# Kernel tuning notes

Measured on AMD Instinct MI355X. Metric: run time of the kernel, lower is better.

The kernel has to match this reference:

```python
import jax, jax.numpy as jnp
import numpy as np

EMBED_DIM = 256
NUM_HEADS = 4
HEAD_DIM = EMBED_DIM // NUM_HEADS
B, H, W = 2, 64, 64


def _conv1x1(x, w, b):
    # x: [B,C,H,W], w: [O,C], b: [O] -> [B,O,H,W]
    return jnp.einsum('oc,bchw->bohw', w, x) + b[None, :, None, None]


def setup_inputs() -> dict:
    key = jax.random.key(0)
    ks = jax.random.split(key, 10)
    s = 1.0 / np.sqrt(EMBED_DIM)
    d = dict(
        x_q=jax.random.normal(ks[0], (B, EMBED_DIM, H, W), jnp.float32),
        x_kv=jax.random.normal(ks[1], (B, EMBED_DIM, H, W), jnp.float32),
        wq=jax.random.normal(ks[2], (EMBED_DIM, EMBED_DIM), jnp.float32) * s,
        bq=jax.random.normal(ks[3], (EMBED_DIM,), jnp.float32) * s,
        wk=jax.random.normal(ks[4], (EMBED_DIM, EMBED_DIM), jnp.float32) * s,
        bk=jax.random.normal(ks[5], (EMBED_DIM,), jnp.float32) * s,
        wv=jax.random.normal(ks[6], (EMBED_DIM, EMBED_DIM), jnp.float32) * s,
        bv=jax.random.normal(ks[7], (EMBED_DIM,), jnp.float32) * s,
        wo=jax.random.normal(ks[8], (EMBED_DIM, EMBED_DIM), jnp.float32) * s,
        bo=jax.random.normal(ks[9], (EMBED_DIM,), jnp.float32) * s,
    )
    return d


def reference(x_q, x_kv, wq, bq, wk, bk, wv, bv, wo, bo):
    b, c, h, w = x_q.shape
    scale = HEAD_DIM ** (-0.5)
    q = _conv1x1(x_q, wq, bq)
    k = _conv1x1(x_kv, wk, bk)
    v = _conv1x1(x_kv, wv, bv)
    s = h * w
    # [B, heads, head_dim, S]
    q = q.reshape(b, NUM_HEADS, HEAD_DIM, s)
    k = k.reshape(b, NUM_HEADS, HEAD_DIM, s)
    v = v.reshape(b, NUM_HEADS, HEAD_DIM, s)
    # attn[b,h,i,j] = sum_d q[b,h,d,i] * k[b,h,d,j]
    attn = jnp.einsum('bndi,bndj->bnij', q, k) * scale
    attn = jax.nn.softmax(attn, axis=-1)
    # out[b,h,i,d] = sum_j attn[b,h,i,j] * v[b,h,d,j]
    out = jnp.einsum('bnij,bndj->bnid', attn, v)
    out = out.transpose(0, 1, 3, 2).reshape(b, c, h, w)
    return _conv1x1(out, wo, bo)
```

## Files before the change

kernel.cpp:

```cpp
#include <hip/hip_runtime.h>
#include <hip/hip_bf16.h>
#include <type_traits>
#include <cstdint>

typedef float  f32x4  __attribute__((ext_vector_type(4)));
typedef short  s16x8  __attribute__((ext_vector_type(8)));
typedef __bf16 bf16x8 __attribute__((ext_vector_type(8)));

#if __has_builtin(__builtin_amdgcn_exp2f)
#define EXP2(x) __builtin_amdgcn_exp2f(x)
#else
#define EXP2(x) exp2f(x)
#endif

template <typename V>
__device__ static inline auto mfma_try(V a, V b, f32x4 c, int)
    -> decltype(__builtin_amdgcn_mfma_f32_16x16x32_bf16(a, b, c, 0, 0, 0)) {
  return __builtin_amdgcn_mfma_f32_16x16x32_bf16(a, b, c, 0, 0, 0);
}
template <typename V>
__device__ static inline f32x4 mfma_try(V a, V b, f32x4 c, long) {
  return __builtin_amdgcn_mfma_f32_16x16x32_bf16(
      __builtin_bit_cast(bf16x8, a), __builtin_bit_cast(bf16x8, b), c, 0, 0, 0);
}
__device__ static inline f32x4 MFMA_BF16(s16x8 a, s16x8 b, f32x4 c) {
  return mfma_try(a, b, c, 0);
}

static constexpr size_t OFF_XTQ  = 0;
static constexpr size_t OFF_XTKV = 2097152;
static constexpr size_t OFF_WQ   = 4194304;
static constexpr size_t OFF_WK   = 4259840;
static constexpr size_t OFF_WV   = 4325376;
static constexpr size_t OFF_WO   = 4390912;
static constexpr size_t OFF_Q    = 4456448;
static constexpr size_t OFF_K    = 6553600;
static constexpr size_t OFF_V    = 8650752;
static constexpr size_t OFF_AO   = 10747904;

__global__ __launch_bounds__(256) void prep_kernel(
    const float* __restrict__ xq, const float* __restrict__ xkv,
    const float* __restrict__ wq, const float* __restrict__ wk,
    const float* __restrict__ wv, const float* __restrict__ wo,
    __bf16* __restrict__ ws) {
  __shared__ __bf16 lds[64 * 66];
  const int t = threadIdx.x;
  const int z = blockIdx.z;
  if (z < 2) {
    const float* src = (z == 0) ? xq : xkv;
    __bf16* dst = ws + ((z == 0) ? OFF_XTQ : OFF_XTKV);
    const int id = blockIdx.x;
    const int b  = id >> 8;
    const int t2 = id & 255;
    const int ct = (t2 & 3) * 64;
    const int st = (t2 >> 2) * 64;
    const float* sb = src + (size_t)b * 1048576;
    __bf16* db = dst + (size_t)b * 1048576;
    const int l = t & 63;
    const int g = t >> 6;
#pragma unroll
    for (int r = 0; r < 16; ++r) {
      const int c = g * 16 + r;
      lds[c * 66 + l] = (__bf16)sb[(size_t)(ct + c) * 4096 + st + l];
    }
    __syncthreads();
#pragma unroll
    for (int r = 0; r < 16; ++r) {
      const int s = g * 16 + r;
      db[(size_t)(st + s) * 256 + ct + l] = lds[l * 66 + s];
    }
  } else {
    const int e0 = blockIdx.x * 512 + t;
#pragma unroll
    for (int p = 0; p < 2; ++p) {
      const int e = e0 + p * 256;
      const int m = e >> 16;
      const int idx = e & 65535;
      const float* w = (m == 0) ? wq : (m == 1) ? wk : (m == 2) ? wv : wo;
      ws[OFF_WQ + (size_t)m * 65536 + idx] = (__bf16)w[idx];
    }
  }
}

__global__ __launch_bounds__(256) void proj_kernel(
    const __bf16* __restrict__ wsr, __bf16* __restrict__ wsw,
    const float* __restrict__ bq, const float* __restrict__ bk,
    const float* __restrict__ bv) {
  __shared__ __align__(16) unsigned char Wl[64 * 512];
  const int z = blockIdx.z;
  const int proj = z >> 1;
  const int b = z & 1;
  const int t = threadIdx.x;
  const int l = t & 63;
  const int w = t >> 6;
  const int lr = l >> 4, lc = l & 15;
  const int bx = blockIdx.x;

  const __bf16* XT = wsr + ((proj == 0) ? OFF_XTQ : OFF_XTKV) + (size_t)b * 1048576;
  const __bf16* W  = wsr + ((proj == 0) ? OFF_WQ : (proj == 1) ? OFF_WK : OFF_WV);
  const float* bias = (proj == 0) ? bq : (proj == 1) ? bk : bv;

  const int otile = (bx & 3) * 64;
#pragma unroll
  for (int p = 0; p < 8; ++p) {
    const int id = p * 256 + t;
    const int row = id >> 5, ch = id & 31;
    *(s16x8*)(Wl + row * 512 + ((ch ^ (row & 7)) * 16)) =
        *(const s16x8*)(W + (size_t)(otile + row) * 256 + ch * 8);
  }
  __syncthreads();
  const int lcx = lc & 7;

  if (proj < 2) {
    const int stile = (bx >> 2) * 128 + w * 32;
    f32x4 acc[2][4];
#pragma unroll
    for (int i = 0; i < 2; ++i)
#pragma unroll
      for (int j = 0; j < 4; ++j) acc[i][j] = f32x4{0.f, 0.f, 0.f, 0.f};
    for (int it = 0; it < 8; ++it) {
      const int c0 = it * 32 + lr * 8;
      s16x8 af[2], bfr[4];
#pragma unroll
      for (int mi = 0; mi < 2; ++mi)
        af[mi] = *(const s16x8*)(XT + (size_t)(stile + mi * 16 + lc) * 256 + c0);
#pragma unroll
      for (int ni = 0; ni < 4; ++ni)
        bfr[ni] = *(const s16x8*)(Wl + (ni * 16 + lc) * 512 + (((it * 4 + lr) ^ lcx) * 16));
#pragma unroll
      for (int mi = 0; mi < 2; ++mi)
#pragma unroll
        for (int ni = 0; ni < 4; ++ni)
          acc[mi][ni] = MFMA_BF16(af[mi], bfr[ni], acc[mi][ni]);
    }
    const float scale = (proj == 0) ? 0.125f * 1.44269504088896f : 1.0f;
    __bf16* dst = wsw + ((proj == 0) ? OFF_Q : OFF_K);
#pragma unroll
    for (int ni = 0; ni < 4; ++ni) {
      const int o = otile + ni * 16 + lc;
      const float bb = bias[o];
      const int n = o >> 6, d = o & 63;
#pragma unroll
      for (int mi = 0; mi < 2; ++mi)
#pragma unroll
        for (int r = 0; r < 4; ++r) {
          const int s = stile + mi * 16 + lr * 4 + r;
          dst[((size_t)(b * 4 + n) * 4096 + s) * 64 + d] =
              (__bf16)((acc[mi][ni][r] + bb) * scale);
        }
    }
  } else {
    const int stile = (bx >> 2) * 128 + w * 32;
    f32x4 acc[4][2];
#pragma unroll
    for (int i = 0; i < 4; ++i)
#pragma unroll
      for (int j = 0; j < 2; ++j) acc[i][j] = f32x4{0.f, 0.f, 0.f, 0.f};
    for (int it = 0; it < 8; ++it) {
      const int c0 = it * 32 + lr * 8;
      s16x8 af[4], bfr[2];
#pragma unroll
      for (int mi = 0; mi < 4; ++mi)
        af[mi] = *(const s16x8*)(Wl + (mi * 16 + lc) * 512 + (((it * 4 + lr) ^ lcx) * 16));
#pragma unroll
      for (int ni = 0; ni < 2; ++ni)
        bfr[ni] = *(const s16x8*)(XT + (size_t)(stile + ni * 16 + lc) * 256 + c0);
#pragma unroll
      for (int mi = 0; mi < 4; ++mi)
#pragma unroll
        for (int ni = 0; ni < 2; ++ni)
          acc[mi][ni] = MFMA_BF16(af[mi], bfr[ni], acc[mi][ni]);
    }
    __bf16* dst = wsw + OFF_V;
#pragma unroll
    for (int mi = 0; mi < 4; ++mi)
#pragma unroll
      for (int r = 0; r < 4; ++r) {
        const int o = otile + mi * 16 + lr * 4 + r;
        const float bb = bias[o];
        const int n = o >> 6, d = o & 63;
#pragma unroll
        for (int ni = 0; ni < 2; ++ni) {
          const int s = stile + ni * 16 + lc;
          dst[((size_t)(b * 4 + n) * 64 + d) * 4096 + s] = (__bf16)(acc[mi][ni][r] + bb);
        }
      }
  }
}

__global__ __launch_bounds__(512) void attn_kernel(
    const __bf16* __restrict__ wsr, __bf16* __restrict__ wsw) {
  __shared__ __align__(16) unsigned char smem[81920];
  unsigned char* const Kb = smem;
  unsigned char* const Vb = smem + 32768;
  unsigned char* const Pb = smem + 65536;
  float* const Mg = (float*)smem;

  const int t = threadIdx.x;
  const int l = t & 63;
  const int w = t >> 6;
  const int g = w >> 2;
  const int wq = w & 3;
  const int lr = l >> 4, lc = l & 15;
  const int bh = blockIdx.y;
  const int qbase = blockIdx.x * 64;

  const __bf16* Q = wsr + OFF_Q + (size_t)bh * (4096 * 64);
  const __bf16* K = wsr + OFF_K + (size_t)bh * (4096 * 64);
  const __bf16* V = wsr + OFF_V + (size_t)bh * (64 * 4096);

  s16x8 aq[2];
#pragma unroll
  for (int kb = 0; kb < 2; ++kb)
    aq[kb] = *(const s16x8*)(Q + (size_t)(qbase + wq * 16 + lc) * 64 + kb * 32 + lr * 8);

  f32x4 o4[4];
#pragma unroll
  for (int i = 0; i < 4; ++i) o4[i] = f32x4{0.f, 0.f, 0.f, 0.f};
  float m = -1e30f, lsum = 0.f;

  unsigned char* const Pw = Pb + w * 2048;
  const int lcx = lc & 7;

  const int srow = t >> 3, sch = t & 7;
  const int soff = srow * 128 + ((sch ^ (srow & 7)) * 16);
  s16x8 pr0, pr1, pr2, pr3;

  {
    pr0 = *(const s16x8*)(K + (size_t)(srow) * 64 + sch * 8);
    pr1 = *(const s16x8*)(K + (size_t)(64 + srow) * 64 + sch * 8);
    pr2 = *(const s16x8*)(V + (size_t)srow * 4096 + sch * 8);
    pr3 = *(const s16x8*)(V + (size_t)srow * 4096 + 64 + sch * 8);
    *(s16x8*)(Kb + soff) = pr0;
    *(s16x8*)(Kb + 16384 + soff) = pr1;
    *(s16x8*)(Vb + soff) = pr2;
    *(s16x8*)(Vb + 16384 + soff) = pr3;
  }
  __syncthreads();

  int cur = 0;
#pragma unroll 1
  for (int it = 0; it < 32; ++it) {
    const bool more = (it + 1 < 32);
    if (more) {
      const int jb0 = (it + 1) * 128;
      pr0 = *(const s16x8*)(K + (size_t)(jb0 + srow) * 64 + sch * 8);
      pr1 = *(const s16x8*)(K + (size_t)(jb0 + 64 + srow) * 64 + sch * 8);
      pr2 = *(const s16x8*)(V + (size_t)srow * 4096 + jb0 + sch * 8);
      pr3 = *(const s16x8*)(V + (size_t)srow * 4096 + jb0 + 64 + sch * 8);
    }

    unsigned char* const kt = Kb + g * 16384 + cur * 8192;
    unsigned char* const vt = Vb + g * 16384 + cur * 8192;

    f32x4 s4[4];
    __builtin_amdgcn_s_setprio(1);
#pragma unroll
    for (int jt = 0; jt < 4; ++jt) {
      f32x4 a = f32x4{0.f, 0.f, 0.f, 0.f};
#pragma unroll
      for (int kb = 0; kb < 2; ++kb) {
        s16x8 bk = *(const s16x8*)(kt + (jt * 16 + lc) * 128 + (((kb * 4 + lr) ^ lcx) * 16));
        a = MFMA_BF16(bk, aq[kb], a);
      }
      s4[jt] = a;
    }
    __builtin_amdgcn_s_setprio(0);

    float pmax = fmaxf(fmaxf(fmaxf(s4[0][0], s4[0][1]), fmaxf(s4[0][2], s4[0][3])),
                       fmaxf(fmaxf(s4[1][0], s4[1][1]), fmaxf(s4[1][2], s4[1][3])));
    pmax = fmaxf(pmax,
                 fmaxf(fmaxf(fmaxf(s4[2][0], s4[2][1]), fmaxf(s4[2][2], s4[2][3])),
                       fmaxf(fmaxf(s4[3][0], s4[3][1]), fmaxf(s4[3][2], s4[3][3]))));
    pmax = fmaxf(pmax, __shfl_xor(pmax, 16));
    pmax = fmaxf(pmax, __shfl_xor(pmax, 32));

    if (!__all(pmax - m <= 12.0f)) {
      const float mn = fmaxf(m, pmax);
      const float f = EXP2(m - mn);
      m = mn;
      lsum *= f;
      float fb[4];
#pragma unroll
      for (int r = 0; r < 4; ++r) fb[r] = __shfl(f, lr * 4 + r);
#pragma unroll
      for (int nt = 0; nt < 4; ++nt)
#pragma unroll
        for (int r = 0; r < 4; ++r) o4[nt][r] *= fb[r];
    }

    float rs = 0.f;
#pragma unroll
    for (int jt = 0; jt < 4; ++jt) {
      union { __bf16 h[4]; unsigned long long u; } pk4;
      float p0 = EXP2(s4[jt][0] - m);
      float p1 = EXP2(s4[jt][1] - m);
      float p2 = EXP2(s4[jt][2] - m);
      float p3 = EXP2(s4[jt][3] - m);
      rs += (p0 + p1) + (p2 + p3);
      pk4.h[0] = (__bf16)p0; pk4.h[1] = (__bf16)p1;
      pk4.h[2] = (__bf16)p2; pk4.h[3] = (__bf16)p3;
      *(unsigned long long*)(Pw + lc * 128 + (((2 * jt + (lr >> 1)) ^ lcx) * 16) + (lr & 1) * 8) = pk4.u;
    }
    rs += __shfl_xor(rs, 16);
    rs += __shfl_xor(rs, 32);
    lsum += rs;

    __builtin_amdgcn_s_setprio(1);
#pragma unroll
    for (int kb = 0; kb < 2; ++kb) {
      s16x8 pa = *(const s16x8*)(Pw + lc * 128 + (((kb * 4 + lr) ^ lcx) * 16));
#pragma unroll
      for (int nt = 0; nt < 4; ++nt) {
        s16x8 bv = *(const s16x8*)(vt + (nt * 16 + lc) * 128 + (((kb * 4 + lr) ^ lcx) * 16));
        o4[nt] = MFMA_BF16(pa, bv, o4[nt]);
      }
    }
    __builtin_amdgcn_s_setprio(0);

    if (more) {
      unsigned char* const kwr = Kb + (cur ^ 1) * 8192;
      unsigned char* const vwr = Vb + (cur ^ 1) * 8192;
      *(s16x8*)(kwr + soff) = pr0;
      *(s16x8*)(kwr + 16384 + soff) = pr1;
      *(s16x8*)(vwr + soff) = pr2;
      *(s16x8*)(vwr + 16384 + soff) = pr3;
    }
    __syncthreads();
    cur ^= 1;
  }

  float m4[4], l4[4];
#pragma unroll
  for (int r = 0; r < 4; ++r) {
    m4[r] = __shfl(m, lr * 4 + r);
    l4[r] = __shfl(lsum, lr * 4 + r);
  }

  if (g == 1) {
#pragma unroll
    for (int nt = 0; nt < 4; ++nt)
#pragma unroll
      for (int r = 0; r < 4; ++r)
        Mg[(wq * 16 + lr * 4 + r) * 66 + nt * 16 + lc] = o4[nt][r];
    if (lc == 0) {
#pragma unroll
      for (int r = 0; r < 4; ++r) {
        Mg[(wq * 16 + lr * 4 + r) * 66 + 64] = m4[r];
        Mg[(wq * 16 + lr * 4 + r) * 66 + 65] = l4[r];
      }
    }
  }
  __syncthreads();
  if (g == 0) {
    const int b = bh >> 2, n = bh & 3;
    __bf16* AO = wsw + OFF_AO + (size_t)b * (4096 * 256);
#pragma unroll
    for (int r = 0; r < 4; ++r) {
      const int row = wq * 16 + lr * 4 + r;
      const float m2 = Mg[row * 66 + 64];
      const float l2 = Mg[row * 66 + 65];
      const float M = fmaxf(m4[r], m2);
      const float f1 = EXP2(m4[r] - M);
      const float f2 = EXP2(m2 - M);
      const float linv = 1.0f / (l4[r] * f1 + l2 * f2);
      const int s = qbase + row;
#pragma unroll
      for (int nt = 0; nt < 4; ++nt) {
        const float val = (o4[nt][r] * f1 + Mg[row * 66 + nt * 16 + lc] * f2) * linv;
        AO[(size_t)s * 256 + n * 64 + nt * 16 + lc] = (__bf16)val;
      }
    }
  }
}

__global__ __launch_bounds__(256) void outproj_kernel(
    const __bf16* __restrict__ wsr, const float* __restrict__ bo,
    float* __restrict__ out) {
  __shared__ __align__(16) unsigned char AOl[64 * 512];
  const int b = blockIdx.y;
  const int bx = blockIdx.x;
  const int t = threadIdx.x;
  const int l = t & 63;
  const int w = t >> 6;
  const int lr = l >> 4, lc = l & 15;
  const int otile = (bx & 1) * 128 + w * 32;
  const int stile = (bx >> 1) * 64;
  const __bf16* Wo = wsr + OFF_WO;
  const __bf16* AO = wsr + OFF_AO + (size_t)b * 1048576;

#pragma unroll
  for (int p = 0; p < 8; ++p) {
    const int id = p * 256 + t;
    const int row = id >> 5, ch = id & 31;
    *(s16x8*)(AOl + row * 512 + ((ch ^ (row & 7)) * 16)) =
        *(const s16x8*)(AO + (size_t)(stile + row) * 256 + ch * 8);
  }
  __syncthreads();
  const int lcx = lc & 7;

  f32x4 acc[2][4];
#pragma unroll
  for (int i = 0; i < 2; ++i)
#pragma unroll
    for (int j = 0; j < 4; ++j) acc[i][j] = f32x4{0.f, 0.f, 0.f, 0.f};

  for (int it = 0; it < 8; ++it) {
    const int c0 = it * 32 + lr * 8;
    s16x8 af[2], bfr[4];
#pragma unroll
    for (int mi = 0; mi < 2; ++mi)
      af[mi] = *(const s16x8*)(Wo + (size_t)(otile + mi * 16 + lc) * 256 + c0);
#pragma unroll
    for (int ni = 0; ni < 4; ++ni)
      bfr[ni] = *(const s16x8*)(AOl + (ni * 16 + lc) * 512 + (((it * 4 + lr) ^ lcx) * 16));
#pragma unroll
    for (int mi = 0; mi < 2; ++mi)
#pragma unroll
      for (int ni = 0; ni < 4; ++ni)
        acc[mi][ni] = MFMA_BF16(af[mi], bfr[ni], acc[mi][ni]);
  }
#pragma unroll
  for (int mi = 0; mi < 2; ++mi)
#pragma unroll
    for (int r = 0; r < 4; ++r) {
      const int o = otile + mi * 16 + lr * 4 + r;
      const float bb = bo[o];
#pragma unroll
      for (int ni = 0; ni < 4; ++ni) {
        const int s = stile + ni * 16 + lc;
        out[((size_t)b * 256 + o) * 4096 + s] = acc[mi][ni][r] + bb;
      }
    }
}

extern "C" void kernel_launch(void* const* d_in, const int* in_sizes, int n_in,
                              void* d_out, int out_size, void* d_ws, size_t ws_size,
                              hipStream_t stream) {
  const float* xq  = (const float*)d_in[0];
  const float* xkv = (const float*)d_in[1];
  const float* wq  = (const float*)d_in[2];
  const float* bq  = (const float*)d_in[3];
  const float* wk  = (const float*)d_in[4];
  const float* bk  = (const float*)d_in[5];
  const float* wv  = (const float*)d_in[6];
  const float* bv  = (const float*)d_in[7];
  const float* wo  = (const float*)d_in[8];
  const float* bo  = (const float*)d_in[9];
  __bf16* ws = (__bf16*)d_ws;
  float* out = (float*)d_out;

  prep_kernel<<<dim3(512, 1, 3), 256, 0, stream>>>(xq, xkv, wq, wk, wv, wo, ws);
  proj_kernel<<<dim3(128, 1, 6), 256, 0, stream>>>(ws, ws, bq, bk, bv);
  attn_kernel<<<dim3(64, 8), 512, 0, stream>>>(ws, ws);
  outproj_kernel<<<dim3(128, 2), 256, 0, stream>>>(ws, bo, out);
}
```

Before: 155.7 us.

## Vectorize prep transpose, unroll GEMM loops, interleave attention grid across heads

```diff
diff --git a/kernel.cpp b/kernel.cpp
--- a/kernel.cpp
+++ b/kernel.cpp
@@ -43,7 +43,7 @@
     const float* __restrict__ wq, const float* __restrict__ wk,
     const float* __restrict__ wv, const float* __restrict__ wo,
     __bf16* __restrict__ ws) {
-  __shared__ __bf16 lds[64 * 66];
+  __shared__ float xl[64 * 67];
   const int t = threadIdx.x;
   const int z = blockIdx.z;
   if (z < 2) {
@@ -56,18 +56,26 @@
     const int st = (t2 >> 2) * 64;
     const float* sb = src + (size_t)b * 1048576;
     __bf16* db = dst + (size_t)b * 1048576;
-    const int l = t & 63;
-    const int g = t >> 6;
-#pragma unroll
-    for (int r = 0; r < 16; ++r) {
-      const int c = g * 16 + r;
-      lds[c * 66 + l] = (__bf16)sb[(size_t)(ct + c) * 4096 + st + l];
+    const int cl = t >> 4;
+    const int sq = t & 15;
+#pragma unroll
+    for (int p = 0; p < 4; ++p) {
+      const int c = cl + p * 16;
+      const f32x4 v = *(const f32x4*)(sb + (size_t)(ct + c) * 4096 + st + sq * 4);
+      xl[(sq * 4 + 0) * 67 + c] = v[0];
+      xl[(sq * 4 + 1) * 67 + c] = v[1];
+      xl[(sq * 4 + 2) * 67 + c] = v[2];
+      xl[(sq * 4 + 3) * 67 + c] = v[3];
     }
     __syncthreads();
 #pragma unroll
-    for (int r = 0; r < 16; ++r) {
-      const int s = g * 16 + r;
-      db[(size_t)(st + s) * 256 + ct + l] = lds[l * 66 + s];
+    for (int q = 0; q < 2; ++q) {
+      const int idq = q * 256 + t;
+      const int s = idq >> 3, ch = idq & 7;
+      union { __bf16 h[8]; s16x8 v; } o;
+#pragma unroll
+      for (int k = 0; k < 8; ++k) o.h[k] = (__bf16)xl[s * 67 + ch * 8 + k];
+      *(s16x8*)(db + (size_t)(st + s) * 256 + ct + ch * 8) = o.v;
     }
   } else {
     const int e0 = blockIdx.x * 512 + t;
@@ -118,6 +126,7 @@
     for (int i = 0; i < 2; ++i)
 #pragma unroll
       for (int j = 0; j < 4; ++j) acc[i][j] = f32x4{0.f, 0.f, 0.f, 0.f};
+#pragma unroll
     for (int it = 0; it < 8; ++it) {
       const int c0 = it * 32 + lr * 8;
       s16x8 af[2], bfr[4];
@@ -156,6 +165,7 @@
     for (int i = 0; i < 4; ++i)
 #pragma unroll
       for (int j = 0; j < 2; ++j) acc[i][j] = f32x4{0.f, 0.f, 0.f, 0.f};
+#pragma unroll
     for (int it = 0; it < 8; ++it) {
       const int c0 = it * 32 + lr * 8;
       s16x8 af[4], bfr[2];
@@ -202,8 +212,8 @@
   const int g = w >> 2;
   const int wq = w & 3;
   const int lr = l >> 4, lc = l & 15;
-  const int bh = blockIdx.y;
-  const int qbase = blockIdx.x * 64;
+  const int bh = blockIdx.x & 7;
+  const int qbase = (blockIdx.x >> 3) * 64;
 
   const __bf16* Q = wsr + OFF_Q + (size_t)bh * (4096 * 64);
   const __bf16* K = wsr + OFF_K + (size_t)bh * (4096 * 64);
@@ -405,6 +415,7 @@
 #pragma unroll
     for (int j = 0; j < 4; ++j) acc[i][j] = f32x4{0.f, 0.f, 0.f, 0.f};
 
+#pragma unroll
   for (int it = 0; it < 8; ++it) {
     const int c0 = it * 32 + lr * 8;
     s16x8 af[2], bfr[4];
@@ -452,6 +463,6 @@
 
   prep_kernel<<<dim3(512, 1, 3), 256, 0, stream>>>(xq, xkv, wq, wk, wv, wo, ws);
   proj_kernel<<<dim3(128, 1, 6), 256, 0, stream>>>(ws, ws, bq, bk, bv);
-  attn_kernel<<<dim3(64, 8), 512, 0, stream>>>(ws, ws);
+  attn_kernel<<<dim3(512), 512, 0, stream>>>(ws, ws);
   outproj_kernel<<<dim3(128, 2), 256, 0, stream>>>(ws, bo, out);
 }
```

New measurement: 154.5 us. No clear change (-0.7%).
